# Kernel tuning notes

Hardware: AMD Instinct MI355X
Metric: run time of the kernel (lower is better)

The kernel has to match this reference:

```python
import jax, jax.numpy as jnp
import numpy as np

D_MODEL = 1024
N_HEADS = 16
D_FF = 4096
EPS = 1e-5


def setup_inputs() -> dict:
    key = jax.random.key(0)
    ks = jax.random.split(key, 16)
    B, S, D, F = 2, 2048, D_MODEL, D_FF
    s_d = 1.0 / np.sqrt(D)
    s_f = 1.0 / np.sqrt(F)
    return {
        "x": jax.random.normal(ks[0], (B, S, D), dtype=jnp.float32),
        "pad_mask": jnp.ones((B, S), dtype=jnp.int32),
        "ln1_g": jnp.ones((D,), jnp.float32), "ln1_b": jnp.zeros((D,), jnp.float32),
        "ln2_g": jnp.ones((D,), jnp.float32), "ln2_b": jnp.zeros((D,), jnp.float32),
        # weights stored [in, out] (equivalent to torch Linear weight.T)
        "wq": jax.random.normal(ks[1], (D, D), jnp.float32) * s_d,
        "bq": jnp.zeros((D,), jnp.float32),
        "wk": jax.random.normal(ks[2], (D, D), jnp.float32) * s_d,
        "bk": jnp.zeros((D,), jnp.float32),
        "wv": jax.random.normal(ks[3], (D, D), jnp.float32) * s_d,
        "bv": jnp.zeros((D,), jnp.float32),
        "wo": jax.random.normal(ks[4], (D, D), jnp.float32) * s_d,
        "bo": jnp.zeros((D,), jnp.float32),
        "w1": jax.random.normal(ks[5], (D, F), jnp.float32) * s_d,
        "b1": jnp.zeros((F,), jnp.float32),
        "w2": jax.random.normal(ks[6], (F, D), jnp.float32) * s_f,
        "b2": jnp.zeros((D,), jnp.float32),
    }


def _layernorm(x, g, b):
    mu = jnp.mean(x, axis=-1, keepdims=True)
    var = jnp.mean(jnp.square(x - mu), axis=-1, keepdims=True)
    return (x - mu) * jax.lax.rsqrt(var + EPS) * g + b


def reference(x, pad_mask, ln1_g, ln1_b, ln2_g, ln2_b,
              wq, bq, wk, bk, wv, bv, wo, bo, w1, b1, w2, b2):
    B, S, D = x.shape
    H = N_HEADS
    dk = D // H

    # mask: causal [1,1,S,S] * pad [B,1,1,S]
    causal = jnp.tril(jnp.ones((S, S), dtype=jnp.int32))[None, None]
    mask = pad_mask[:, None, None, :] * causal  # [B,1,S,S]

    h = _layernorm(x, ln1_g, ln1_b)
    q = (h @ wq + bq).reshape(B, S, H, dk).transpose(0, 2, 1, 3)
    k = (h @ wk + bk).reshape(B, S, H, dk).transpose(0, 2, 1, 3)
    v = (h @ wv + bv).reshape(B, S, H, dk).transpose(0, 2, 1, 3)

    scores = jnp.einsum('bhqd,bhkd->bhqk', q, k) / np.sqrt(dk)
    scores = jnp.where(mask == 0, -jnp.inf, scores)
    attn = jax.nn.softmax(scores, axis=-1)
    ctx = jnp.einsum('bhqk,bhkd->bhqd', attn, v)
    ctx = ctx.transpose(0, 2, 1, 3).reshape(B, S, D)
    x = x + ctx @ wo + bo

    h2 = _layernorm(x, ln2_g, ln2_b)
    ff = jax.nn.gelu(h2 @ w1 + b1, approximate=False) @ w2 + b2
    return x + ff
```

## Files before the change

### kernel.cpp

```cpp
#include <hip/hip_runtime.h>
#include <math.h>


typedef unsigned short bfu;
typedef unsigned short u16x4 __attribute__((ext_vector_type(4)));
typedef unsigned short u16x8 __attribute__((ext_vector_type(8)));
typedef __bf16         bf16x8 __attribute__((ext_vector_type(8)));
typedef float          f32x4 __attribute__((ext_vector_type(4)));

#define SEQ   2048
#define NTOK  4096
#define DM    1024
#define DKH   64

static __device__ __forceinline__ float bfu2f(bfu u) {
  return __uint_as_float(((unsigned)u) << 16);
}
static __device__ __forceinline__ bfu f2bfu(float f) {
  unsigned u = __float_as_uint(f);
  u += 0x7FFFu + ((u >> 16) & 1u);
  return (bfu)(u >> 16);
}
static __device__ __forceinline__ float ldF(const void* p, size_t i, bool isbf) {
  return isbf ? bfu2f(((const bfu*)p)[i]) : ((const float*)p)[i];
}
static __device__ __forceinline__ bool dt_isbf(const void* dt) {
  return *(const unsigned*)dt == 0x3F803F80u;
}
static __device__ __forceinline__ void g2l16(const void* g, void* l) {
  __builtin_amdgcn_global_load_lds((const __attribute__((address_space(1))) void*)g,
                                   (__attribute__((address_space(3))) void*)l,
                                   16, 0, 0);
}

static __device__ __forceinline__ void tr_tile(const void* in, bfu* out,
                                               int R, int C, int gx, int gy,
                                               bool isbf, bfu t[64][65]) {
  const int tx = threadIdx.x & 63, ty = threadIdx.x >> 6;
#pragma unroll
  for (int i = 0; i < 16; ++i) {
    int rr = i * 4 + ty;
    size_t idx = (size_t)(gy + rr) * C + gx + tx;
    t[rr][tx] = isbf ? ((const bfu*)in)[idx] : f2bfu(((const float*)in)[idx]);
  }
  __syncthreads();
#pragma unroll
  for (int i = 0; i < 16; ++i) {
    int cc = i * 4 + ty;
    out[(size_t)(gx + cc) * R + gy + tx] = t[tx][cc];
  }
}

__global__ __launch_bounds__(256) void prep_k(
    const void* ln1g, const void* ln1b, const void* ln2g, const void* ln2b,
    const void* bq, const void* bk, const void* bv, const void* bo,
    const void* b1, const void* b2,
    const void* wq, const void* wk, const void* wv, const void* wo,
    const void* w1, const void* w2,
    bfu* __restrict__ vecs, bfu* __restrict__ wqkvT, bfu* __restrict__ woT,
    bfu* __restrict__ w1T, bfu* __restrict__ w2T) {
  __shared__ bfu t[64][65];
  const bool isbf = dt_isbf(ln1g);
  const int bid = blockIdx.x, tid = threadIdx.x;
  if (bid < 52) {
    const void* src; int segStart, segDst;
    if      (bid < 4)  { src = ln1g; segStart = 0;  segDst = 0; }
    else if (bid < 8)  { src = ln1b; segStart = 4;  segDst = 1024; }
    else if (bid < 12) { src = ln2g; segStart = 8;  segDst = 2048; }
    else if (bid < 16) { src = ln2b; segStart = 12; segDst = 3072; }
    else if (bid < 20) { src = bq;   segStart = 16; segDst = 4096; }
    else if (bid < 24) { src = bk;   segStart = 20; segDst = 5120; }
    else if (bid < 28) { src = bv;   segStart = 24; segDst = 6144; }
    else if (bid < 32) { src = bo;   segStart = 28; segDst = 7168; }
    else if (bid < 48) { src = b1;   segStart = 32; segDst = 8192; }
    else               { src = b2;   segStart = 48; segDst = 12288; }
    const int off = (bid - segStart) * 256 + tid;
    vecs[segDst + off] = isbf ? ((const bfu*)src)[off]
                              : f2bfu(((const float*)src)[off]);
    return;
  }
  const void* in; bfu* out; int R, C, gx, gy;
  const int j = bid - 52;
  if (j < 1024) {
    const int mat = j >> 8, rem = j & 255;
    in  = (mat == 0) ? wq : (mat == 1) ? wk : (mat == 2) ? wv : wo;
    out = (mat == 0) ? wqkvT : (mat == 1) ? wqkvT + 1048576
        : (mat == 2) ? wqkvT + 2097152 : woT;
    R = 1024; C = 1024; gx = (rem & 15) * 64; gy = (rem >> 4) * 64;
  } else if (j < 2048) {
    const int rem = j - 1024;
    in = w1; out = w1T; R = 1024; C = 4096;
    gx = (rem & 63) * 64; gy = (rem >> 6) * 64;
  } else {
    const int rem = j - 2048;
    in = w2; out = w2T; R = 4096; C = 1024;
    gx = (rem & 15) * 64; gy = (rem >> 4) * 64;
  }
  tr_tile(in, out, R, C, gx, gy, isbf, t);
}

__global__ __launch_bounds__(256) void trw2_k(const void* __restrict__ w2,
                                              bfu* __restrict__ out,
                                              const void* __restrict__ dt) {
  __shared__ bfu t[64][65];
  const bool isbf = dt_isbf(dt);
  const int rem = blockIdx.x;
  tr_tile(w2, out, 4096, 1024, (rem & 15) * 64, (rem >> 4) * 64, isbf, t);
}

template <bool RAW>
__global__ __launch_bounds__(256) void ln_k(const void* __restrict__ xin,
                                            const bfu* __restrict__ g,
                                            const bfu* __restrict__ bb,
                                            bfu* __restrict__ y,
                                            const void* __restrict__ dt) {
  const int t = threadIdx.x;
  const size_t base = (size_t)blockIdx.x * DM;
  const int c0 = t * 4;
  float v[4];
  bool isbf = true;
  if constexpr (RAW) isbf = dt_isbf(dt);
  if (!RAW || isbf) {
    u16x4 u = *(const u16x4*)((const bfu*)xin + base + c0);
#pragma unroll
    for (int i = 0; i < 4; ++i) v[i] = bfu2f(u[i]);
  } else {
    float4 f = *(const float4*)((const float*)xin + base + c0);
    v[0] = f.x; v[1] = f.y; v[2] = f.z; v[3] = f.w;
  }
  float s1 = v[0] + v[1] + v[2] + v[3];
  float s2 = v[0]*v[0] + v[1]*v[1] + v[2]*v[2] + v[3]*v[3];
#pragma unroll
  for (int o = 32; o; o >>= 1) {
    s1 += __shfl_xor(s1, o);
    s2 += __shfl_xor(s2, o);
  }
  __shared__ float r1[4], r2[4];
  const int wid = t >> 6, lane = t & 63;
  if (lane == 0) { r1[wid] = s1; r2[wid] = s2; }
  __syncthreads();
  s1 = r1[0] + r1[1] + r1[2] + r1[3];
  s2 = r2[0] + r2[1] + r2[2] + r2[3];
  const float mu = s1 * (1.0f / DM);
  const float var = s2 * (1.0f / DM) - mu * mu;
  const float rs = rsqrtf(var + 1e-5f);
  u16x4 gv = *(const u16x4*)&g[c0];
  u16x4 bv = *(const u16x4*)&bb[c0];
  u16x4 ov;
#pragma unroll
  for (int i = 0; i < 4; ++i)
    ov[i] = f2bfu((v[i] - mu) * rs * bfu2f(gv[i]) + bfu2f(bv[i]));
  *(u16x4*)&y[base + c0] = ov;
}

template <int EPI, int BM>
__global__ __launch_bounds__(256) void gemm_bt(const bfu* __restrict__ A,
                                               const bfu* __restrict__ Bt,
                                               const bfu* __restrict__ bias,
                                               const void* __restrict__ res,
                                               void* __restrict__ C,
                                               int M, int N, int K,
                                               const void* __restrict__ dt) {
  constexpr int NF = (BM == 128) ? 4 : 2;
  __shared__ __align__(16) bfu Asm[BM * 32];
  __shared__ __align__(16) bfu Bsm[128 * 32];
  const bool isbf = dt_isbf(dt);
  const int tid = threadIdx.x;
  const int m0 = blockIdx.y * BM, n0 = blockIdx.x * 128;
  const int wid = tid >> 6, lane = tid & 63;
  const int wm = (BM == 128) ? (wid >> 1) * 64 : 0;
  const int wn = (BM == 128) ? (wid & 1) * 64 : wid * 32;
  const int quad = lane >> 4, l16 = lane & 15;

  f32x4 acc[4][NF] = {};

  const int c0 = tid, c1 = tid + 256;
  const bfu* agp0 = A + (size_t)(m0 + (c0 >> 2)) * K + (c0 & 3) * 8;
  const bfu* agp1 = A + (size_t)(m0 + ((c1 >> 2) & (BM - 1))) * K + (c1 & 3) * 8;
  const bfu* bgp0 = Bt + (size_t)(n0 + (c0 >> 2)) * K + (c0 & 3) * 8;
  const bfu* bgp1 = Bt + (size_t)(n0 + (c1 >> 2)) * K + (c1 & 3) * 8;
  bfu* al0 = Asm + c0 * 8;
  bfu* al1 = Asm + (BM == 128 ? c1 * 8 : 0);
  bfu* bl0 = Bsm + c0 * 8;
  bfu* bl1 = Bsm + c1 * 8;

  for (int k0 = 0; k0 < K; k0 += 32) {
    g2l16(agp0 + k0, al0);
    if constexpr (BM == 128) g2l16(agp1 + k0, al1);
    g2l16(bgp0 + k0, bl0);
    g2l16(bgp1 + k0, bl1);
    __syncthreads();

    u16x8 af[4], bfr[NF];
#pragma unroll
    for (int i = 0; i < 4; ++i)
      af[i] = *(const u16x8*)&Asm[(wm + i * 16 + l16) * 32 + quad * 8];
#pragma unroll
    for (int i = 0; i < NF; ++i)
      bfr[i] = *(const u16x8*)&Bsm[(wn + i * 16 + l16) * 32 + quad * 8];
#pragma unroll
    for (int mi = 0; mi < 4; ++mi)
#pragma unroll
      for (int ni = 0; ni < NF; ++ni)
        acc[mi][ni] = __builtin_amdgcn_mfma_f32_16x16x32_bf16(
            __builtin_bit_cast(bf16x8, af[mi]),
            __builtin_bit_cast(bf16x8, bfr[ni]), acc[mi][ni], 0, 0, 0);
    __syncthreads();
  }

#pragma unroll
  for (int mi = 0; mi < 4; ++mi) {
#pragma unroll
    for (int ni = 0; ni < NF; ++ni) {
      const int col = n0 + wn + ni * 16 + l16;
      const float bvv = bfu2f(bias[col]);
#pragma unroll
      for (int r = 0; r < 4; ++r) {
        const int row = m0 + wm + mi * 16 + quad * 4 + r;
        const size_t idx = (size_t)row * N + col;
        float v = acc[mi][ni][r] + bvv;
        if constexpr (EPI == 1) {
          v = 0.5f * v * (1.0f + erff(v * 0.70710678118f));
          ((bfu*)C)[idx] = f2bfu(v);
        } else if constexpr (EPI == 2) {
          v += ldF(res, idx, isbf);
          ((bfu*)C)[idx] = f2bfu(v);
        } else if constexpr (EPI == 3) {
          v += bfu2f(((const bfu*)res)[idx]);
          if (isbf) ((bfu*)C)[idx] = f2bfu(v);
          else      ((float*)C)[idx] = v;
        } else {
          ((bfu*)C)[idx] = f2bfu(v);
        }
      }
    }
  }
}

#define NEG_BIG (-1e30f)
#define KSTR 72

__global__ __launch_bounds__(256) void attn_flash(const bfu* __restrict__ qkv,
                                                  const int* __restrict__ pad,
                                                  bfu* __restrict__ ctx) {
  __shared__ __align__(16) bfu Kb[64 * KSTR];
  __shared__ __align__(16) bfu VT[64 * KSTR];
  __shared__ __align__(16) bfu Pb[4][16 * KSTR];

  const int tid = threadIdx.x;
  const int wid = tid >> 6, lane = tid & 63;
  const int quad = lane >> 4, l16 = lane & 15;
  const int bh = blockIdx.x;
  const int b = bh >> 4, h = bh & 15;
  const int q0 = blockIdx.y * 64;

  const bfu* qptr = qkv + (size_t)(b * SEQ + q0 + wid * 16 + l16) * 3072 + h * 64 + quad * 8;
  u16x8 qfr[2];
#pragma unroll
  for (int kt = 0; kt < 2; ++kt) {
    u16x8 qr = *(const u16x8*)(qptr + kt * 32);
#pragma unroll
    for (int j = 0; j < 8; ++j) qr[j] = f2bfu(bfu2f(qr[j]) * 0.125f);
    qfr[kt] = qr;
  }

  f32x4 Ofr[4] = {};
  float mrow[4], lrow[4];
#pragma unroll
  for (int r = 0; r < 4; ++r) { mrow[r] = NEG_BIG; lrow[r] = 0.0f; }

  const bfu* kvbase = qkv + (size_t)(b * SEQ) * 3072 + h * 64;
  const int* pb = pad + b * SEQ;
  const int qrow_base = q0 + wid * 16 + quad * 4;

  const int ntiles = q0 / 64 + 1;
  for (int t = 0; t < ntiles; ++t) {
    const int k0 = t * 64;
    __syncthreads();

#pragma unroll
    for (int s = 0; s < 2; ++s) {
      const int cc = tid + s * 256;
      const int key = cc >> 3, pc = cc & 7;
      u16x8 kv8 = *(const u16x8*)(kvbase + (size_t)(k0 + key) * 3072 + 1024 + pc * 8);
      *(u16x8*)&Kb[key * KSTR + pc * 8] = kv8;
    }
    {
      const int vkey = tid & 63, dblk = tid >> 6;
      const bfu* vp = kvbase + (size_t)(k0 + vkey) * 3072 + 2048 + dblk * 16;
      u16x8 v0 = *(const u16x8*)vp;
      u16x8 v1 = *(const u16x8*)(vp + 8);
#pragma unroll
      for (int j = 0; j < 8; ++j) VT[(dblk * 16 + j) * KSTR + vkey] = v0[j];
#pragma unroll
      for (int j = 0; j < 8; ++j) VT[(dblk * 16 + 8 + j) * KSTR + vkey] = v1[j];
    }
    __syncthreads();

    f32x4 S[4] = {};
#pragma unroll
    for (int nt = 0; nt < 4; ++nt) {
#pragma unroll
      for (int kt = 0; kt < 2; ++kt) {
        u16x8 bf = *(const u16x8*)&Kb[(nt * 16 + l16) * KSTR + kt * 32 + quad * 8];
        S[nt] = __builtin_amdgcn_mfma_f32_16x16x32_bf16(
            __builtin_bit_cast(bf16x8, qfr[kt]),
            __builtin_bit_cast(bf16x8, bf), S[nt], 0, 0, 0);
      }
    }

    float p[4][4];
    float cmax[4] = {NEG_BIG, NEG_BIG, NEG_BIG, NEG_BIG};
#pragma unroll
    for (int nt = 0; nt < 4; ++nt) {
      const int key = k0 + nt * 16 + l16;
      const bool ok = (pb[key] != 0);
#pragma unroll
      for (int r = 0; r < 4; ++r) {
        float s = (ok && key <= qrow_base + r) ? S[nt][r] : NEG_BIG;
        p[nt][r] = s;
        cmax[r] = fmaxf(cmax[r], s);
      }
    }
#pragma unroll
    for (int off = 1; off < 16; off <<= 1)
#pragma unroll
      for (int r = 0; r < 4; ++r) cmax[r] = fmaxf(cmax[r], __shfl_xor(cmax[r], off));
    float alpha[4];
#pragma unroll
    for (int r = 0; r < 4; ++r) {
      const float mn = fmaxf(mrow[r], cmax[r]);
      alpha[r] = __expf(mrow[r] - mn);
      mrow[r] = mn;
    }
    float psum[4] = {0, 0, 0, 0};
#pragma unroll
    for (int nt = 0; nt < 4; ++nt)
#pragma unroll
      for (int r = 0; r < 4; ++r) {
        p[nt][r] = __expf(p[nt][r] - mrow[r]);
        psum[r] += p[nt][r];
      }
#pragma unroll
    for (int off = 1; off < 16; off <<= 1)
#pragma unroll
      for (int r = 0; r < 4; ++r) psum[r] += __shfl_xor(psum[r], off);
#pragma unroll
    for (int r = 0; r < 4; ++r) lrow[r] = lrow[r] * alpha[r] + psum[r];
#pragma unroll
    for (int n = 0; n < 4; ++n)
#pragma unroll
      for (int r = 0; r < 4; ++r) Ofr[n][r] *= alpha[r];

#pragma unroll
    for (int nt = 0; nt < 4; ++nt)
#pragma unroll
      for (int r = 0; r < 4; ++r)
        Pb[wid][(quad * 4 + r) * KSTR + nt * 16 + l16] = f2bfu(p[nt][r]);
    __syncthreads();

#pragma unroll
    for (int at = 0; at < 2; ++at) {
      u16x8 af = *(const u16x8*)&Pb[wid][l16 * KSTR + at * 32 + quad * 8];
#pragma unroll
      for (int n = 0; n < 4; ++n) {
        u16x8 bf = *(const u16x8*)&VT[(n * 16 + l16) * KSTR + at * 32 + quad * 8];
        Ofr[n] = __builtin_amdgcn_mfma_f32_16x16x32_bf16(
            __builtin_bit_cast(bf16x8, af),
            __builtin_bit_cast(bf16x8, bf), Ofr[n], 0, 0, 0);
      }
    }
  }

  float inv[4];
#pragma unroll
  for (int r = 0; r < 4; ++r) inv[r] = 1.0f / lrow[r];
#pragma unroll
  for (int n = 0; n < 4; ++n)
#pragma unroll
    for (int r = 0; r < 4; ++r)
      ctx[(size_t)(b * SEQ + qrow_base + r) * DM + h * 64 + n * 16 + l16] =
          f2bfu(Ofr[n][r] * inv[r]);
}

extern "C" void kernel_launch(void* const* d_in, const int* in_sizes, int n_in,
                              void* d_out, int out_size, void* d_ws, size_t ws_size,
                              hipStream_t stream) {
  (void)in_sizes; (void)n_in; (void)out_size;
  const void* x    = d_in[0];
  const int*  pad  = (const int*)d_in[1];
  const void* ln1g = d_in[2];
  const void* ln1b = d_in[3];
  const void* ln2g = d_in[4];
  const void* ln2b = d_in[5];
  const void* wq   = d_in[6];
  const void* bq   = d_in[7];
  const void* wk   = d_in[8];
  const void* bk   = d_in[9];
  const void* wv   = d_in[10];
  const void* bv   = d_in[11];
  const void* wo   = d_in[12];
  const void* bo   = d_in[13];
  const void* w1   = d_in[14];
  const void* b1   = d_in[15];
  const void* w2   = d_in[16];
  const void* b2   = d_in[17];

  const bool flat = ws_size >= (size_t)(37765120 + 1024) * 2;
  bfu* base  = (bfu*)d_ws;
  bfu* vecs  = base;
  bfu* wqkvT = vecs  + 16384;
  bfu* woT   = wqkvT + 3145728;
  bfu* w1T   = woT   + 1048576;
  bfu* w2Tf  = w1T   + 4194304;
  bfu* h     = w2Tf  + (flat ? 4194304 : 0);
  bfu* qkv   = h     + 4194304;
  bfu* ctx   = qkv   + 12582912;
  bfu* x1    = ctx   + 4194304;
  bfu* ffh   = qkv;
  bfu* w2T   = flat ? w2Tf : h;

  const dim3 blk(256);
  bfu* lg1 = vecs;        bfu* lb1 = vecs + 1024;
  bfu* lg2 = vecs + 2048; bfu* lb2 = vecs + 3072;
  bfu* bqkv = vecs + 4096;
  bfu* boc  = vecs + 7168;
  bfu* b1c  = vecs + 8192;
  bfu* b2c  = vecs + 12288;

  prep_k<<<dim3(flat ? 3124 : 2100), blk, 0, stream>>>(
      ln1g, ln1b, ln2g, ln2b, bq, bk, bv, bo, b1, b2,
      wq, wk, wv, wo, w1, w2, vecs, wqkvT, woT, w1T, w2T);

  ln_k<true><<<dim3(NTOK), blk, 0, stream>>>(x, lg1, lb1, h, ln1g);
  gemm_bt<0, 128><<<dim3(24, 32), blk, 0, stream>>>(h, wqkvT, bqkv, nullptr,
                                                    qkv, NTOK, 3072, 1024, ln1g);
  attn_flash<<<dim3(32, 32), blk, 0, stream>>>(qkv, pad, ctx);
  gemm_bt<2, 64><<<dim3(8, 64), blk, 0, stream>>>(ctx, woT, boc, x, x1,
                                                  NTOK, 1024, 1024, ln1g);
  ln_k<false><<<dim3(NTOK), blk, 0, stream>>>(x1, lg2, lb2, h, ln1g);
  gemm_bt<1, 128><<<dim3(32, 32), blk, 0, stream>>>(h, w1T, b1c, nullptr, ffh,
                                                    NTOK, 4096, 1024, ln1g);
  if (!flat) trw2_k<<<dim3(1024), blk, 0, stream>>>(w2, w2T, ln1g);
  gemm_bt<3, 64><<<dim3(8, 64), blk, 0, stream>>>(ffh, w2T, b2c, x1, d_out,
                                                  NTOK, 1024, 4096, ln1g);
}
```

Before: 472.7 us.

## Enlarge flash-attention query tile to 128 rows with balanced causal tile ordering

Each attention block now handles 128 query rows, 32 per wavefront in two MFMA row fragments. This halves K/V global loads and LDS staging per query row and halves the grid. Block y indices are remapped so long and short causal tiles interleave, and the causal mask comparison is skipped on tiles fully below the diagonal. The __syncthreads before the P·V step is removed because each wavefront only reads its own P buffer. The trade-off is higher register pressure and fewer blocks, which may lower occupancy.

```diff
diff --git a/kernel.cpp b/kernel.cpp
--- a/kernel.cpp
+++ b/kernel.cpp
@@ -245,35 +245,42 @@
                                                   bfu* __restrict__ ctx) {
   __shared__ __align__(16) bfu Kb[64 * KSTR];
   __shared__ __align__(16) bfu VT[64 * KSTR];
-  __shared__ __align__(16) bfu Pb[4][16 * KSTR];
+  __shared__ __align__(16) bfu Pb[4][32 * KSTR];
 
   const int tid = threadIdx.x;
   const int wid = tid >> 6, lane = tid & 63;
   const int quad = lane >> 4, l16 = lane & 15;
   const int bh = blockIdx.x;
   const int b = bh >> 4, h = bh & 15;
-  const int q0 = blockIdx.y * 64;
-
-  const bfu* qptr = qkv + (size_t)(b * SEQ + q0 + wid * 16 + l16) * 3072 + h * 64 + quad * 8;
-  u16x8 qfr[2];
-#pragma unroll
-  for (int kt = 0; kt < 2; ++kt) {
-    u16x8 qr = *(const u16x8*)(qptr + kt * 32);
-#pragma unroll
-    for (int j = 0; j < 8; ++j) qr[j] = f2bfu(bfu2f(qr[j]) * 0.125f);
-    qfr[kt] = qr;
-  }
-
-  f32x4 Ofr[4] = {};
-  float mrow[4], lrow[4];
-#pragma unroll
-  for (int r = 0; r < 4; ++r) { mrow[r] = NEG_BIG; lrow[r] = 0.0f; }
+  const int yq = blockIdx.y;
+  const int qt = (yq < 8) ? yq : 23 - yq;
+  const int q0 = qt * 128;
+
+  u16x8 qfr[2][2];
+#pragma unroll
+  for (int mf = 0; mf < 2; ++mf) {
+    const bfu* qp = qkv + (size_t)(b * SEQ + q0 + wid * 32 + mf * 16 + l16) * 3072
+                    + h * 64 + quad * 8;
+#pragma unroll
+    for (int kt = 0; kt < 2; ++kt) {
+      u16x8 qr = *(const u16x8*)(qp + kt * 32);
+#pragma unroll
+      for (int j = 0; j < 8; ++j) qr[j] = f2bfu(bfu2f(qr[j]) * 0.125f);
+      qfr[mf][kt] = qr;
+    }
+  }
+
+  f32x4 Ofr[2][4] = {};
+  float mrow[2][4], lrow[2][4];
+#pragma unroll
+  for (int mf = 0; mf < 2; ++mf)
+#pragma unroll
+    for (int r = 0; r < 4; ++r) { mrow[mf][r] = NEG_BIG; lrow[mf][r] = 0.0f; }
 
   const bfu* kvbase = qkv + (size_t)(b * SEQ) * 3072 + h * 64;
   const int* pb = pad + b * SEQ;
-  const int qrow_base = q0 + wid * 16 + quad * 4;
-
-  const int ntiles = q0 / 64 + 1;
+
+  const int ntiles = 2 * qt + 2;
   for (int t = 0; t < ntiles; ++t) {
     const int k0 = t * 64;
     __syncthreads();
@@ -297,90 +304,102 @@
     }
     __syncthreads();
 
-    f32x4 S[4] = {};
-#pragma unroll
-    for (int nt = 0; nt < 4; ++nt) {
-#pragma unroll
-      for (int kt = 0; kt < 2; ++kt) {
-        u16x8 bf = *(const u16x8*)&Kb[(nt * 16 + l16) * KSTR + kt * 32 + quad * 8];
-        S[nt] = __builtin_amdgcn_mfma_f32_16x16x32_bf16(
-            __builtin_bit_cast(bf16x8, qfr[kt]),
-            __builtin_bit_cast(bf16x8, bf), S[nt], 0, 0, 0);
+    const bool edge = (k0 + 64 > q0);
+
+#pragma unroll
+    for (int mf = 0; mf < 2; ++mf) {
+      f32x4 S[4] = {};
+#pragma unroll
+      for (int nt = 0; nt < 4; ++nt)
+#pragma unroll
+        for (int kt = 0; kt < 2; ++kt) {
+          u16x8 bf = *(const u16x8*)&Kb[(nt * 16 + l16) * KSTR + kt * 32 + quad * 8];
+          S[nt] = __builtin_amdgcn_mfma_f32_16x16x32_bf16(
+              __builtin_bit_cast(bf16x8, qfr[mf][kt]),
+              __builtin_bit_cast(bf16x8, bf), S[nt], 0, 0, 0);
+        }
+
+      const int qrb = q0 + wid * 32 + mf * 16 + quad * 4;
+      float p[4][4];
+      float cmax[4] = {NEG_BIG, NEG_BIG, NEG_BIG, NEG_BIG};
+#pragma unroll
+      for (int nt = 0; nt < 4; ++nt) {
+        const int key = k0 + nt * 16 + l16;
+        const bool ok = (pb[key] != 0);
+#pragma unroll
+        for (int r = 0; r < 4; ++r) {
+          float s = (ok && (!edge || key <= qrb + r)) ? S[nt][r] : NEG_BIG;
+          p[nt][r] = s;
+          cmax[r] = fmaxf(cmax[r], s);
+        }
       }
+#pragma unroll
+      for (int off = 1; off < 16; off <<= 1)
+#pragma unroll
+        for (int r = 0; r < 4; ++r)
+          cmax[r] = fmaxf(cmax[r], __shfl_xor(cmax[r], off));
+      float alpha[4];
+#pragma unroll
+      for (int r = 0; r < 4; ++r) {
+        const float mn = fmaxf(mrow[mf][r], cmax[r]);
+        alpha[r] = __expf(mrow[mf][r] - mn);
+        mrow[mf][r] = mn;
+      }
+      float psum[4] = {0, 0, 0, 0};
+#pragma unroll
+      for (int nt = 0; nt < 4; ++nt)
+#pragma unroll
+        for (int r = 0; r < 4; ++r) {
+          p[nt][r] = __expf(p[nt][r] - mrow[mf][r]);
+          psum[r] += p[nt][r];
+        }
+#pragma unroll
+      for (int off = 1; off < 16; off <<= 1)
+#pragma unroll
+        for (int r = 0; r < 4; ++r) psum[r] += __shfl_xor(psum[r], off);
+#pragma unroll
+      for (int r = 0; r < 4; ++r)
+        lrow[mf][r] = lrow[mf][r] * alpha[r] + psum[r];
+#pragma unroll
+      for (int n = 0; n < 4; ++n)
+#pragma unroll
+        for (int r = 0; r < 4; ++r) Ofr[mf][n][r] *= alpha[r];
+
+#pragma unroll
+      for (int nt = 0; nt < 4; ++nt)
+#pragma unroll
+        for (int r = 0; r < 4; ++r)
+          Pb[wid][(mf * 16 + quad * 4 + r) * KSTR + nt * 16 + l16] = f2bfu(p[nt][r]);
     }
 
-    float p[4][4];
-    float cmax[4] = {NEG_BIG, NEG_BIG, NEG_BIG, NEG_BIG};
-#pragma unroll
-    for (int nt = 0; nt < 4; ++nt) {
-      const int key = k0 + nt * 16 + l16;
-      const bool ok = (pb[key] != 0);
-#pragma unroll
-      for (int r = 0; r < 4; ++r) {
-        float s = (ok && key <= qrow_base + r) ? S[nt][r] : NEG_BIG;
-        p[nt][r] = s;
-        cmax[r] = fmaxf(cmax[r], s);
+#pragma unroll
+    for (int mf = 0; mf < 2; ++mf)
+#pragma unroll
+      for (int at = 0; at < 2; ++at) {
+        u16x8 af = *(const u16x8*)&Pb[wid][(mf * 16 + l16) * KSTR + at * 32 + quad * 8];
+#pragma unroll
+        for (int n = 0; n < 4; ++n) {
+          u16x8 bf = *(const u16x8*)&VT[(n * 16 + l16) * KSTR + at * 32 + quad * 8];
+          Ofr[mf][n] = __builtin_amdgcn_mfma_f32_16x16x32_bf16(
+              __builtin_bit_cast(bf16x8, af),
+              __builtin_bit_cast(bf16x8, bf), Ofr[mf][n], 0, 0, 0);
+        }
       }
-    }
-#pragma unroll
-    for (int off = 1; off < 16; off <<= 1)
-#pragma unroll
-      for (int r = 0; r < 4; ++r) cmax[r] = fmaxf(cmax[r], __shfl_xor(cmax[r], off));
-    float alpha[4];
-#pragma unroll
-    for (int r = 0; r < 4; ++r) {
-      const float mn = fmaxf(mrow[r], cmax[r]);
-      alpha[r] = __expf(mrow[r] - mn);
-      mrow[r] = mn;
-    }
-    float psum[4] = {0, 0, 0, 0};
-#pragma unroll
-    for (int nt = 0; nt < 4; ++nt)
-#pragma unroll
-      for (int r = 0; r < 4; ++r) {
-        p[nt][r] = __expf(p[nt][r] - mrow[r]);
-        psum[r] += p[nt][r];
-      }
-#pragma unroll
-    for (int off = 1; off < 16; off <<= 1)
-#pragma unroll
-      for (int r = 0; r < 4; ++r) psum[r] += __shfl_xor(psum[r], off);
-#pragma unroll
-    for (int r = 0; r < 4; ++r) lrow[r] = lrow[r] * alpha[r] + psum[r];
+  }
+
+#pragma unroll
+  for (int mf = 0; mf < 2; ++mf) {
+    const int qrb = q0 + wid * 32 + mf * 16 + quad * 4;
+    float inv[4];
+#pragma unroll
+    for (int r = 0; r < 4; ++r) inv[r] = 1.0f / lrow[mf][r];
 #pragma unroll
     for (int n = 0; n < 4; ++n)
 #pragma unroll
-      for (int r = 0; r < 4; ++r) Ofr[n][r] *= alpha[r];
-
-#pragma unroll
-    for (int nt = 0; nt < 4; ++nt)
-#pragma unroll
       for (int r = 0; r < 4; ++r)
-        Pb[wid][(quad * 4 + r) * KSTR + nt * 16 + l16] = f2bfu(p[nt][r]);
-    __syncthreads();
-
-#pragma unroll
-    for (int at = 0; at < 2; ++at) {
-      u16x8 af = *(const u16x8*)&Pb[wid][l16 * KSTR + at * 32 + quad * 8];
-#pragma unroll
-      for (int n = 0; n < 4; ++n) {
-        u16x8 bf = *(const u16x8*)&VT[(n * 16 + l16) * KSTR + at * 32 + quad * 8];
-        Ofr[n] = __builtin_amdgcn_mfma_f32_16x16x32_bf16(
-            __builtin_bit_cast(bf16x8, af),
-            __builtin_bit_cast(bf16x8, bf), Ofr[n], 0, 0, 0);
-      }
-    }
-  }
-
-  float inv[4];
-#pragma unroll
-  for (int r = 0; r < 4; ++r) inv[r] = 1.0f / lrow[r];
-#pragma unroll
-  for (int n = 0; n < 4; ++n)
-#pragma unroll
-    for (int r = 0; r < 4; ++r)
-      ctx[(size_t)(b * SEQ + qrow_base + r) * DM + h * 64 + n * 16 + l16] =
-          f2bfu(Ofr[n][r] * inv[r]);
+        ctx[(size_t)(b * SEQ + qrb + r) * DM + h * 64 + n * 16 + l16] =
+            f2bfu(Ofr[mf][n][r] * inv[r]);
+  }
 }
 
 extern "C" void kernel_launch(void* const* d_in, const int* in_sizes, int n_in,
@@ -435,7 +454,7 @@
   ln_k<true><<<dim3(NTOK), blk, 0, stream>>>(x, lg1, lb1, h, ln1g);
   gemm_bt<0, 128><<<dim3(24, 32), blk, 0, stream>>>(h, wqkvT, bqkv, nullptr,
                                                     qkv, NTOK, 3072, 1024, ln1g);
-  attn_flash<<<dim3(32, 32), blk, 0, stream>>>(qkv, pad, ctx);
+  attn_flash<<<dim3(32, 16), blk, 0, stream>>>(qkv, pad, ctx);
   gemm_bt<2, 64><<<dim3(8, 64), blk, 0, stream>>>(ctx, woT, boc, x, x1,
                                                   NTOK, 1024, 1024, ln1g);
   ln_k<false><<<dim3(NTOK), blk, 0, stream>>>(x1, lg2, lb2, h, ln1g);
```

Result: slower. 532.8 us (+12.7%).
